# Performance work log

Hardware: AMD Instinct MI355X
Metric: run time of the kernel (lower is better)

The kernel has to match this reference:

```python
import jax, jax.numpy as jnp
import numpy as np

N, H, W = 128, 64, 64
CH_I, CH_H, CH_Q = 2, 150, 10
N_ACT = 8


def conv3x3(x, w):
    # x: [N,H,W,Cin], w: [3,3,Cin,Cout], 'same' padding, stride 1
    return jax.lax.conv_general_dilated(
        x, w, window_strides=(1, 1), padding='SAME',
        dimension_numbers=('NHWC', 'HWIO', 'NHWC'))


def setup_inputs() -> dict:
    key = jax.random.key(0)
    ks = jax.random.split(key, 9)
    std = 0.01
    x = jax.random.normal(ks[0], (N, H, W, CH_I), dtype=jnp.float32)
    S1 = jax.random.randint(ks[1], (N,), 0, H, dtype=jnp.int32)
    S2 = jax.random.randint(ks[2], (N,), 0, W, dtype=jnp.int32)
    w0 = std * jax.random.normal(ks[3], (3, 3, CH_I, CH_H), dtype=jnp.float32)
    b0 = jnp.zeros((CH_H,), dtype=jnp.float32)
    w_r = std * jax.random.normal(ks[4], (3, 3, CH_H, 1), dtype=jnp.float32)
    w_q = std * jax.random.normal(ks[5], (3, 3, 2, CH_Q), dtype=jnp.float32)
    w_sw = std * jax.random.normal(ks[6], (3, 3, 2, CH_Q), dtype=jnp.float32)
    w_sw2 = std * jax.random.normal(ks[7], (3, 3, 2, CH_Q), dtype=jnp.float32)
    w_dense = std * jax.random.normal(ks[8], (CH_Q, N_ACT), dtype=jnp.float32)
    return {"x": x, "S1": S1, "S2": S2, "VInum": 36,
            "w0": w0, "b0": b0, "w_r": w_r, "w_q": w_q,
            "w_sw": w_sw, "w_sw2": w_sw2, "w_dense": w_dense}


def reference(x, S1, S2, VInum, w0, b0, w_r, w_q, w_sw, w_sw2, w_dense):
    k = int(VInum)
    h = conv3x3(x, w0) + b0                      # [N,H,W,ch_h]
    r = conv3x3(h, w_r)                          # [N,H,W,1] reward map
    v = jnp.zeros_like(r)
    # first VI step uses conv2 weights
    q = conv3x3(jnp.concatenate([r, v], axis=3), w_q)
    v = jnp.max(q, axis=3, keepdims=True)
    # k-1 shared-weight value-iteration steps
    def body(v, _):
        q = conv3x3(jnp.concatenate([r, v], axis=3), w_sw)
        return jnp.max(q, axis=3, keepdims=True), None
    v, _ = jax.lax.scan(body, v, None, length=k - 1)
    # final step with second shared-weight conv
    q = conv3x3(jnp.concatenate([r, v], axis=3), w_sw2)  # [N,H,W,ch_q]
    # attention: gather Q values at state (S1,S2) per batch element
    q_out = q[jnp.arange(q.shape[0]), S1, S2]            # [N,ch_q]
    logits = q_out @ w_dense                             # [N,8]
    prob_actions = jax.nn.softmax(logits, axis=-1)
    return (logits, prob_actions, q, q_out)
```

## Files before the change

kernel.cpp:

```cpp
#include <hip/hip_runtime.h>
#include <math.h>


typedef float v2f __attribute__((ext_vector_type(2)));

static __device__ __forceinline__ v2f splat2(float s) { v2f r; r.x = s; r.y = s; return r; }
static __device__ __forceinline__ v2f pkfma(v2f w, float v, v2f a) {
#if __has_builtin(__builtin_elementwise_fma)
    return __builtin_elementwise_fma(w, splat2(v), a);
#else
    v2f r; r.x = fmaf(w.x, v, a.x); r.y = fmaf(w.y, v, a.y); return r;
#endif
}
static __device__ __forceinline__ v2f pkmax(v2f a, v2f b) {
#if __has_builtin(__builtin_elementwise_max)
    return __builtin_elementwise_max(a, b);
#else
    v2f r; r.x = fmaxf(a.x, b.x); r.y = fmaxf(a.y, b.y); return r;
#endif
}

#define DPP_SHR1 0x138
#define DPP_SHL1 0x130
template <int CTRL>
static __device__ __forceinline__ float dppsh(float v) {
    return __int_as_float(__builtin_amdgcn_update_dpp(
        0, __float_as_int(v), CTRL, 0xF, 0xF, false));
}

#define XROW 69
#define RROW 68

__global__ void
__attribute__((amdgpu_flat_work_group_size(1024, 1024)))
__attribute__((amdgpu_waves_per_eu(4, 4)))
vin_kernel(const float* __restrict__ x,
           const int* __restrict__ S1,
           const int* __restrict__ S2,
           const int* __restrict__ VInum,
           const float* __restrict__ w0,
           const float* __restrict__ b0,
           const float* __restrict__ w_r,
           const float* __restrict__ w_q,
           const float* __restrict__ w_sw,
           const float* __restrict__ w_sw2,
           const float* __restrict__ w_dense,
           float* __restrict__ out) {
    const int b = blockIdx.x;
    const int t = threadIdx.x;

    __shared__ float xs0[68 * XROW];
    __shared__ float xs1[68 * XROW];
    __shared__ float rs[66 * RROW];
    __shared__ float wtA[1620];
    __shared__ float Pp[450];
    __shared__ float Bt[90];
    __shared__ float Bv[9];
    __shared__ float W5c[459];
    __shared__ float exT[2][17][64];
    __shared__ float exB[2][17][64];
    __shared__ float qsel[10];

    for (int i = t; i < 68 * XROW; i += 1024) { xs0[i] = 0.f; xs1[i] = 0.f; }
    for (int i = t; i < 66 * RROW; i += 1024) rs[i] = 0.f;
    for (int i = t; i < 2 * 17 * 64; i += 1024) {
        ((float*)exT)[i] = 0.f; ((float*)exB)[i] = 0.f;
    }
    if (t < 450) Pp[t] = 0.f;
    __syncthreads();

    const int row = t >> 4;
    const int cb  = (t & 15) << 2;

    {
        const float* xb = x + (size_t)b * 64 * 64 * 2;
        const float4* xp = (const float4*)(xb + (row * 64 + cb) * 2);
        #pragma unroll
        for (int g = 0; g < 2; ++g) {
            float4 v4 = xp[g];
            int px = cb + g * 2;
            xs0[(row + 2) * XROW + px + 2] = v4.x;
            xs1[(row + 2) * XROW + px + 2] = v4.y;
            xs0[(row + 2) * XROW + px + 3] = v4.z;
            xs1[(row + 2) * XROW + px + 3] = v4.w;
        }
    }
    for (int idx = t; idx < 1620; idx += 1024) {
        int entry = idx / 10, ch = idx - entry * 10;
        int d = entry / 18, rem = entry % 18;
        int uu = rem >> 1, ci = rem & 1;
        int c0 = ch * 15;
        const float* wr = w_r + d * 150;
        const float* wp = w0 + (uu * 2 + ci) * 150;
        float s = 0.f;
        for (int c = c0; c < c0 + 15; ++c) s += wr[c] * wp[c];
        wtA[idx] = s;
    }
    if (t < 90) {
        int d = t / 10, ch = t - d * 10, c0 = ch * 15;
        float s = 0.f;
        for (int c = c0; c < c0 + 15; ++c) s += w_r[d * 150 + c] * b0[c];
        Bt[t] = s;
    }
    __syncthreads();
    if (t < 162) {
        float s = 0.f;
        #pragma unroll
        for (int i = 0; i < 10; ++i) s += wtA[t * 10 + i];
        int d = t / 18, rem = t % 18;
        int uu = rem >> 1, ci = rem & 1;
        int dy = d / 3 - 1, dx = d % 3 - 1;
        int uy = uu / 3 - 1, ux = uu % 3 - 1;
        int eidx = (dy + uy + 2) * 5 + (dx + ux + 2);
        Pp[d * 50 + eidx * 2 + ci] = s;
    } else if (t >= 256 && t < 265) {
        int d = t - 256;
        float s = 0.f;
        #pragma unroll
        for (int i = 0; i < 10; ++i) s += Bt[d * 10 + i];
        Bv[d] = s;
    }
    __syncthreads();
    if (t < 459) {
        int cls = t / 51, j = t - cls * 51;
        int cy = cls / 3, cx = cls % 3;
        float s = 0.f;
        #pragma unroll
        for (int d = 0; d < 9; ++d) {
            int dy = d / 3 - 1, dx = d % 3 - 1;
            bool ok = (cy == 0 || (cy == 1 ? dy >= 0 : dy <= 0)) &&
                      (cx == 0 || (cx == 1 ? dx >= 0 : dx <= 0));
            if (ok) s += (j < 50) ? Pp[d * 50 + j] : Bv[d];
        }
        W5c[t] = s;
    }
    __syncthreads();

    {
        int cy = (row == 0) ? 1 : (row == 63) ? 2 : 0;
        #pragma unroll
        for (int p = 0; p < 4; ++p) {
            int xx = cb + p;
            int cx = (xx == 0) ? 1 : (xx == 63) ? 2 : 0;
            const float* Wp = &W5c[(cy * 3 + cx) * 51];
            float acc = Wp[50];
            #pragma unroll
            for (int e = 0; e < 25; ++e) {
                int xi = (row + e / 5) * XROW + (xx + e % 5);
                acc = fmaf(xs0[xi], Wp[e * 2], acc);
                acc = fmaf(xs1[xi], Wp[e * 2 + 1], acc);
            }
            rs[(row + 1) * RROW + xx + 2] = acc;
        }
    }
    __syncthreads();

    const int c  = t & 63;
    const int w  = t >> 6;
    const int r0 = w << 2;
    const int upSlot = (w == 0)  ? 16 : w - 1;
    const int dnSlot = (w == 15) ? 16 : w + 1;
    const int K = VInum[0];

    v2f Rsw2[4][5];
    float vprev[4];
    float RC[6], RL[6], RR[6];
    #pragma unroll
    for (int j = 0; j < 6; ++j) RC[j] = rs[(r0 + j) * RROW + c + 2];
    #pragma unroll
    for (int j = 0; j < 6; ++j) { RL[j] = dppsh<DPP_SHR1>(RC[j]); RR[j] = dppsh<DPP_SHL1>(RC[j]); }
    {
        float vmax[4];
        #pragma unroll
        for (int a = 0; a < 10; ++a) {
            #pragma unroll
            for (int i = 0; i < 4; ++i) {
                float accR = 0.f, accQ = 0.f;
                #pragma unroll
                for (int d = 0; d < 9; ++d) {
                    const int dy = d / 3, dx = d % 3;
                    const float rv = (dx == 0 ? RL : dx == 1 ? RC : RR)[i + dy];
                    accR = fmaf(w_sw[d * 20 + a], rv, accR);
                    accQ = fmaf(w_q[d * 20 + a],  rv, accQ);
                }
                if (a & 1) Rsw2[i][a >> 1].y = accR; else Rsw2[i][a >> 1].x = accR;
                vmax[i] = (a == 0) ? accQ : fmaxf(vmax[i], accQ);
            }
        }
        exT[1][w][c] = vmax[0];
        exB[1][w][c] = vmax[3];
        #pragma unroll
        for (int i = 0; i < 4; ++i) vprev[i] = vmax[i];
    }
    __syncthreads();

    const float* wsv = w_sw + 10;
    for (int k = 2; k <= K; ++k) {
        const int pr = (k - 1) & 1, pw = k & 1;
        float VC[6], VL[6], VR[6];
        VC[0] = exB[pr][upSlot][c];
        VC[5] = exT[pr][dnSlot][c];
        #pragma unroll
        for (int i = 0; i < 4; ++i) VC[i + 1] = vprev[i];
        #pragma unroll
        for (int j = 0; j < 6; ++j) { VL[j] = dppsh<DPP_SHR1>(VC[j]); VR[j] = dppsh<DPP_SHL1>(VC[j]); }

        v2f acc[4][5];
        #pragma unroll
        for (int ap = 0; ap < 5; ++ap) {
            #pragma unroll
            for (int d = 0; d < 9; ++d) {
                v2f w2; w2.x = wsv[d * 20 + 2 * ap]; w2.y = wsv[d * 20 + 2 * ap + 1];
                const int dy = d / 3, dx = d % 3;
                const float* S = (dx == 0) ? VL : (dx == 1) ? VC : VR;
                #pragma unroll
                for (int i = 0; i < 4; ++i)
                    acc[i][ap] = (d == 0) ? pkfma(w2, S[i + dy], Rsw2[i][ap])
                                          : pkfma(w2, S[i + dy], acc[i][ap]);
            }
        }
        float vnew[4];
        #pragma unroll
        for (int i = 0; i < 4; ++i) {
            v2f m2 = acc[i][0];
            #pragma unroll
            for (int ap = 1; ap < 5; ++ap) m2 = pkmax(m2, acc[i][ap]);
            vnew[i] = fmaxf(m2.x, m2.y);
        }
        exT[pw][w][c] = vnew[0];
        exB[pw][w][c] = vnew[3];
        #pragma unroll
        for (int i = 0; i < 4; ++i) vprev[i] = vnew[i];
        __syncthreads();
    }

    const int s1 = S1[b], s2 = S2[b];
    {
        const int pK = K & 1;
        float VC[6], VL[6], VR[6];
        VC[0] = exB[pK][upSlot][c];
        VC[5] = exT[pK][dnSlot][c];
        #pragma unroll
        for (int i = 0; i < 4; ++i) VC[i + 1] = vprev[i];
        #pragma unroll
        for (int j = 0; j < 6; ++j) { VL[j] = dppsh<DPP_SHR1>(VC[j]); VR[j] = dppsh<DPP_SHL1>(VC[j]); }

        float qv[4][10];
        #pragma unroll
        for (int a = 0; a < 10; ++a) {
            #pragma unroll
            for (int i = 0; i < 4; ++i) {
                float acc = 0.f;
                #pragma unroll
                for (int d = 0; d < 9; ++d) {
                    const int dy = d / 3, dx = d % 3;
                    acc = fmaf(w_sw2[d * 20 + a],
                               (dx == 0 ? RL : dx == 1 ? RC : RR)[i + dy], acc);
                    acc = fmaf(w_sw2[d * 20 + 10 + a],
                               (dx == 0 ? VL : dx == 1 ? VC : VR)[i + dy], acc);
                }
                qv[i][a] = acc;
            }
        }
        #pragma unroll
        for (int i = 0; i < 4; ++i) {
            float2* qp = (float2*)(out + 2048 +
                          ((size_t)((b * 64 + r0 + i) * 64 + c)) * 10);
            #pragma unroll
            for (int g = 0; g < 5; ++g)
                qp[g] = make_float2(qv[i][2 * g], qv[i][2 * g + 1]);
        }
        if (c == s2) {
            #pragma unroll
            for (int i = 0; i < 4; ++i)
                if (s1 == r0 + i) {
                    #pragma unroll
                    for (int a = 0; a < 10; ++a) qsel[a] = qv[i][a];
                }
        }
    }
    __syncthreads();

    if (t == 0) {
        float logits[8];
        float m = -1e30f;
        #pragma unroll
        for (int j = 0; j < 8; ++j) {
            float s = 0.f;
            #pragma unroll
            for (int a = 0; a < 10; ++a) s += qsel[a] * w_dense[a * 8 + j];
            logits[j] = s;
            m = fmaxf(m, s);
        }
        float sum = 0.f;
        float e[8];
        #pragma unroll
        for (int j = 0; j < 8; ++j) { e[j] = expf(logits[j] - m); sum += e[j]; }
        float inv = 1.f / sum;
        #pragma unroll
        for (int j = 0; j < 8; ++j) {
            out[b * 8 + j] = logits[j];
            out[1024 + b * 8 + j] = e[j] * inv;
        }
    }
    if (t < 10) out[5244928 + b * 10 + t] = qsel[t];
}

extern "C" void kernel_launch(void* const* d_in, const int* in_sizes, int n_in,
                              void* d_out, int out_size, void* d_ws, size_t ws_size,
                              hipStream_t stream) {
    const float* x      = (const float*)d_in[0];
    const int*   S1     = (const int*)d_in[1];
    const int*   S2     = (const int*)d_in[2];
    const int*   VInum  = (const int*)d_in[3];
    const float* w0     = (const float*)d_in[4];
    const float* b0     = (const float*)d_in[5];
    const float* w_r    = (const float*)d_in[6];
    const float* w_q    = (const float*)d_in[7];
    const float* w_sw   = (const float*)d_in[8];
    const float* w_sw2  = (const float*)d_in[9];
    const float* w_dense= (const float*)d_in[10];
    float* out = (float*)d_out;

    vin_kernel<<<128, 1024, 0, stream>>>(x, S1, S2, VInum, w0, b0, w_r, w_q,
                                         w_sw, w_sw2, w_dense, out);
}
```

Before: 171.4 us.

## Halve block size to 512 threads, 8 rows per thread, weights in registers

Each thread now computes 8 rows of the value-iteration map instead of 4, with 512 threads per block and 2 waves per SIMD. This lowers the halo overhead per row (shared-memory exchange and DPP shifts) and means fewer waves take part in each per-iteration barrier. The shared-weight conv weights are also loaded once into 45 packed register pairs rather than re-read from memory on every iteration. In exchange, fewer resident waves are left to hide latency, and register pressure rises a lot, which could cause spills.

After: 176.2 us. 1.03x slower.

```diff
diff --git a/kernel.cpp b/kernel.cpp
--- a/kernel.cpp
+++ b/kernel.cpp
@@ -32,8 +32,8 @@
 #define RROW 68
 
 __global__ void
-__attribute__((amdgpu_flat_work_group_size(1024, 1024)))
-__attribute__((amdgpu_waves_per_eu(4, 4)))
+__attribute__((amdgpu_flat_work_group_size(512, 512)))
+__attribute__((amdgpu_waves_per_eu(2, 2)))
 vin_kernel(const float* __restrict__ x,
            const int* __restrict__ S1,
            const int* __restrict__ S2,
@@ -57,26 +57,26 @@
     __shared__ float Bt[90];
     __shared__ float Bv[9];
     __shared__ float W5c[459];
-    __shared__ float exT[2][17][64];
-    __shared__ float exB[2][17][64];
+    __shared__ float exT[2][9][64];
+    __shared__ float exB[2][9][64];
     __shared__ float qsel[10];
 
-    for (int i = t; i < 68 * XROW; i += 1024) { xs0[i] = 0.f; xs1[i] = 0.f; }
-    for (int i = t; i < 66 * RROW; i += 1024) rs[i] = 0.f;
-    for (int i = t; i < 2 * 17 * 64; i += 1024) {
+    for (int i = t; i < 68 * XROW; i += 512) { xs0[i] = 0.f; xs1[i] = 0.f; }
+    for (int i = t; i < 66 * RROW; i += 512) rs[i] = 0.f;
+    for (int i = t; i < 2 * 9 * 64; i += 512) {
         ((float*)exT)[i] = 0.f; ((float*)exB)[i] = 0.f;
     }
     if (t < 450) Pp[t] = 0.f;
     __syncthreads();
 
-    const int row = t >> 4;
-    const int cb  = (t & 15) << 2;
+    const int row = t >> 3;
+    const int cb  = (t & 7) << 3;
 
     {
         const float* xb = x + (size_t)b * 64 * 64 * 2;
         const float4* xp = (const float4*)(xb + (row * 64 + cb) * 2);
         #pragma unroll
-        for (int g = 0; g < 2; ++g) {
+        for (int g = 0; g < 4; ++g) {
             float4 v4 = xp[g];
             int px = cb + g * 2;
             xs0[(row + 2) * XROW + px + 2] = v4.x;
@@ -85,7 +85,7 @@
             xs1[(row + 2) * XROW + px + 3] = v4.w;
         }
     }
-    for (int idx = t; idx < 1620; idx += 1024) {
+    for (int idx = t; idx < 1620; idx += 512) {
         int entry = idx / 10, ch = idx - entry * 10;
         int d = entry / 18, rem = entry % 18;
         int uu = rem >> 1, ci = rem & 1;
@@ -139,7 +139,7 @@
     {
         int cy = (row == 0) ? 1 : (row == 63) ? 2 : 0;
         #pragma unroll
-        for (int p = 0; p < 4; ++p) {
+        for (int p = 0; p < 8; ++p) {
             int xx = cb + p;
             int cx = (xx == 0) ? 1 : (xx == 63) ? 2 : 0;
             const float* Wp = &W5c[(cy * 3 + cx) * 51];
@@ -157,24 +157,26 @@
 
     const int c  = t & 63;
     const int w  = t >> 6;
-    const int r0 = w << 2;
-    const int upSlot = (w == 0)  ? 16 : w - 1;
-    const int dnSlot = (w == 15) ? 16 : w + 1;
+    const int r0 = w << 3;
+    const int upSlot = (w == 0) ? 8 : w - 1;
+    const int dnSlot = (w == 7) ? 8 : w + 1;
     const int K = VInum[0];
 
-    v2f Rsw2[4][5];
-    float vprev[4];
-    float RC[6], RL[6], RR[6];
-    #pragma unroll
-    for (int j = 0; j < 6; ++j) RC[j] = rs[(r0 + j) * RROW + c + 2];
-    #pragma unroll
-    for (int j = 0; j < 6; ++j) { RL[j] = dppsh<DPP_SHR1>(RC[j]); RR[j] = dppsh<DPP_SHL1>(RC[j]); }
+    v2f Rsw2[8][5];
+    float vprev[8];
     {
-        float vmax[4];
+        float RC[10], RL[10], RR[10];
+        #pragma unroll
+        for (int j = 0; j < 10; ++j) RC[j] = rs[(r0 + j) * RROW + c + 2];
+        #pragma unroll
+        for (int j = 0; j < 10; ++j) {
+            RL[j] = dppsh<DPP_SHR1>(RC[j]); RR[j] = dppsh<DPP_SHL1>(RC[j]);
+        }
+        float vmax[8];
         #pragma unroll
         for (int a = 0; a < 10; ++a) {
             #pragma unroll
-            for (int i = 0; i < 4; ++i) {
+            for (int i = 0; i < 8; ++i) {
                 float accR = 0.f, accQ = 0.f;
                 #pragma unroll
                 for (int d = 0; d < 9; ++d) {
@@ -188,68 +190,108 @@
             }
         }
         exT[1][w][c] = vmax[0];
-        exB[1][w][c] = vmax[3];
-        #pragma unroll
-        for (int i = 0; i < 4; ++i) vprev[i] = vmax[i];
-    }
-    __syncthreads();
-
-    const float* wsv = w_sw + 10;
+        exB[1][w][c] = vmax[7];
+        #pragma unroll
+        for (int i = 0; i < 8; ++i) vprev[i] = vmax[i];
+    }
+
+    v2f wv[45];
+    #pragma unroll
+    for (int i = 0; i < 45; ++i) {
+        const int d = i / 5, ap = i - d * 5;
+        v2f v; v.x = w_sw[d * 20 + 10 + 2 * ap]; v.y = w_sw[d * 20 + 10 + 2 * ap + 1];
+        asm volatile("" : "+v"(v));
+        wv[i] = v;
+    }
+    __syncthreads();
+
     for (int k = 2; k <= K; ++k) {
         const int pr = (k - 1) & 1, pw = k & 1;
-        float VC[6], VL[6], VR[6];
+        float VC[10], VL[10], VR[10];
         VC[0] = exB[pr][upSlot][c];
-        VC[5] = exT[pr][dnSlot][c];
-        #pragma unroll
-        for (int i = 0; i < 4; ++i) VC[i + 1] = vprev[i];
-        #pragma unroll
-        for (int j = 0; j < 6; ++j) { VL[j] = dppsh<DPP_SHR1>(VC[j]); VR[j] = dppsh<DPP_SHL1>(VC[j]); }
-
-        v2f acc[4][5];
-        #pragma unroll
-        for (int ap = 0; ap < 5; ++ap) {
-            #pragma unroll
-            for (int d = 0; d < 9; ++d) {
-                v2f w2; w2.x = wsv[d * 20 + 2 * ap]; w2.y = wsv[d * 20 + 2 * ap + 1];
-                const int dy = d / 3, dx = d % 3;
-                const float* S = (dx == 0) ? VL : (dx == 1) ? VC : VR;
-                #pragma unroll
-                for (int i = 0; i < 4; ++i)
-                    acc[i][ap] = (d == 0) ? pkfma(w2, S[i + dy], Rsw2[i][ap])
-                                          : pkfma(w2, S[i + dy], acc[i][ap]);
-            }
-        }
-        float vnew[4];
-        #pragma unroll
-        for (int i = 0; i < 4; ++i) {
-            v2f m2 = acc[i][0];
-            #pragma unroll
-            for (int ap = 1; ap < 5; ++ap) m2 = pkmax(m2, acc[i][ap]);
-            vnew[i] = fmaxf(m2.x, m2.y);
+        VC[9] = exT[pr][dnSlot][c];
+        #pragma unroll
+        for (int i = 0; i < 8; ++i) VC[i + 1] = vprev[i];
+        #pragma unroll
+        for (int j = 0; j < 10; ++j) {
+            VL[j] = dppsh<DPP_SHR1>(VC[j]); VR[j] = dppsh<DPP_SHL1>(VC[j]);
+        }
+
+        float vnew[8];
+        {
+            v2f acc[4][5];
+            #pragma unroll
+            for (int ap = 0; ap < 5; ++ap) {
+                #pragma unroll
+                for (int d = 0; d < 9; ++d) {
+                    const int dy = d / 3, dx = d % 3;
+                    const float* S = (dx == 0) ? VL : (dx == 1) ? VC : VR;
+                    v2f w2 = wv[d * 5 + ap];
+                    #pragma unroll
+                    for (int i = 0; i < 4; ++i)
+                        acc[i][ap] = (d == 0) ? pkfma(w2, S[i + dy], Rsw2[i][ap])
+                                              : pkfma(w2, S[i + dy], acc[i][ap]);
+                }
+            }
+            #pragma unroll
+            for (int i = 0; i < 4; ++i) {
+                v2f m2 = acc[i][0];
+                #pragma unroll
+                for (int ap = 1; ap < 5; ++ap) m2 = pkmax(m2, acc[i][ap]);
+                vnew[i] = fmaxf(m2.x, m2.y);
+            }
+        }
+        {
+            v2f acc[4][5];
+            #pragma unroll
+            for (int ap = 0; ap < 5; ++ap) {
+                #pragma unroll
+                for (int d = 0; d < 9; ++d) {
+                    const int dy = d / 3, dx = d % 3;
+                    const float* S = (dx == 0) ? VL : (dx == 1) ? VC : VR;
+                    v2f w2 = wv[d * 5 + ap];
+                    #pragma unroll
+                    for (int i = 0; i < 4; ++i)
+                        acc[i][ap] = (d == 0) ? pkfma(w2, S[i + 4 + dy], Rsw2[i + 4][ap])
+                                              : pkfma(w2, S[i + 4 + dy], acc[i][ap]);
+                }
+            }
+            #pragma unroll
+            for (int i = 0; i < 4; ++i) {
+                v2f m2 = acc[i][0];
+                #pragma unroll
+                for (int ap = 1; ap < 5; ++ap) m2 = pkmax(m2, acc[i][ap]);
+                vnew[i + 4] = fmaxf(m2.x, m2.y);
+            }
         }
         exT[pw][w][c] = vnew[0];
-        exB[pw][w][c] = vnew[3];
-        #pragma unroll
-        for (int i = 0; i < 4; ++i) vprev[i] = vnew[i];
+        exB[pw][w][c] = vnew[7];
+        #pragma unroll
+        for (int i = 0; i < 8; ++i) vprev[i] = vnew[i];
         __syncthreads();
     }
 
     const int s1 = S1[b], s2 = S2[b];
     {
         const int pK = K & 1;
-        float VC[6], VL[6], VR[6];
+        float RC[10], RL[10], RR[10], VC[10], VL[10], VR[10];
+        #pragma unroll
+        for (int j = 0; j < 10; ++j) RC[j] = rs[(r0 + j) * RROW + c + 2];
         VC[0] = exB[pK][upSlot][c];
-        VC[5] = exT[pK][dnSlot][c];
-        #pragma unroll
-        for (int i = 0; i < 4; ++i) VC[i + 1] = vprev[i];
-        #pragma unroll
-        for (int j = 0; j < 6; ++j) { VL[j] = dppsh<DPP_SHR1>(VC[j]); VR[j] = dppsh<DPP_SHL1>(VC[j]); }
-
-        float qv[4][10];
+        VC[9] = exT[pK][dnSlot][c];
+        #pragma unroll
+        for (int i = 0; i < 8; ++i) VC[i + 1] = vprev[i];
+        #pragma unroll
+        for (int j = 0; j < 10; ++j) {
+            RL[j] = dppsh<DPP_SHR1>(RC[j]); RR[j] = dppsh<DPP_SHL1>(RC[j]);
+            VL[j] = dppsh<DPP_SHR1>(VC[j]); VR[j] = dppsh<DPP_SHL1>(VC[j]);
+        }
+
+        float qv[8][10];
         #pragma unroll
         for (int a = 0; a < 10; ++a) {
             #pragma unroll
-            for (int i = 0; i < 4; ++i) {
+            for (int i = 0; i < 8; ++i) {
                 float acc = 0.f;
                 #pragma unroll
                 for (int d = 0; d < 9; ++d) {
@@ -263,7 +305,7 @@
             }
         }
         #pragma unroll
-        for (int i = 0; i < 4; ++i) {
+        for (int i = 0; i < 8; ++i) {
             float2* qp = (float2*)(out + 2048 +
                           ((size_t)((b * 64 + r0 + i) * 64 + c)) * 10);
             #pragma unroll
@@ -272,7 +314,7 @@
         }
         if (c == s2) {
             #pragma unroll
-            for (int i = 0; i < 4; ++i)
+            for (int i = 0; i < 8; ++i)
                 if (s1 == r0 + i) {
                     #pragma unroll
                     for (int a = 0; a < 10; ++a) qsel[a] = qv[i][a];
@@ -322,6 +364,6 @@
     const float* w_dense= (const float*)d_in[10];
     float* out = (float*)d_out;
 
-    vin_kernel<<<128, 1024, 0, stream>>>(x, S1, S2, VInum, w0, b0, w_r, w_q,
-                                         w_sw, w_sw2, w_dense, out);
-}
+    vin_kernel<<<128, 512, 0, stream>>>(x, S1, S2, VInum, w0, b0, w_r, w_q,
+                                        w_sw, w_sw2, w_dense, out);
+}
```

## Fuse two value-iteration steps per barrier using two-row halo recomputation

Applied to the files above, without the earlier changes.

Each wave now exchanges a two-row halo, packed as float2, and computes two VI steps per synchronization. It first computes 6 rows (its own 4 plus one redundant halo row on each side), then the 4 owned rows from those, which halves the number of __syncthreads barriers in the iterative loop. The price is roughly 50% redundant FMA work in the first step of each pair and more live registers (6x5 precomputed reward terms, 6-row accumulators). Per-action accumulation is split into chunks to limit register pressure, and an odd leftover step is handled separately.

Measured after the change: 183.0 us. 1.07x slower.

```diff
diff --git a/kernel.cpp b/kernel.cpp
--- a/kernel.cpp
+++ b/kernel.cpp
@@ -49,22 +49,23 @@
     const int b = blockIdx.x;
     const int t = threadIdx.x;
 
-    __shared__ float xs0[68 * XROW];
-    __shared__ float xs1[68 * XROW];
-    __shared__ float rs[66 * RROW];
-    __shared__ float wtA[1620];
-    __shared__ float Pp[450];
-    __shared__ float Bt[90];
-    __shared__ float Bv[9];
-    __shared__ float W5c[459];
-    __shared__ float exT[2][17][64];
-    __shared__ float exB[2][17][64];
-    __shared__ float qsel[10];
+    __shared__ float  xs0[68 * XROW];
+    __shared__ float  xs1[68 * XROW];
+    __shared__ float  rs[66 * RROW];
+    __shared__ float  wtA[1620];
+    __shared__ float  Pp[450];
+    __shared__ float  Bt[90];
+    __shared__ float  Bv[9];
+    __shared__ float  W5c[459];
+    __shared__ float2 exU[2][17][64];
+    __shared__ float2 exD[2][17][64];
+    __shared__ float  qsel[10];
 
     for (int i = t; i < 68 * XROW; i += 1024) { xs0[i] = 0.f; xs1[i] = 0.f; }
     for (int i = t; i < 66 * RROW; i += 1024) rs[i] = 0.f;
     for (int i = t; i < 2 * 17 * 64; i += 1024) {
-        ((float*)exT)[i] = 0.f; ((float*)exB)[i] = 0.f;
+        ((float2*)exU)[i] = make_float2(0.f, 0.f);
+        ((float2*)exD)[i] = make_float2(0.f, 0.f);
     }
     if (t < 450) Pp[t] = 0.f;
     __syncthreads();
@@ -162,89 +163,260 @@
     const int dnSlot = (w == 15) ? 16 : w + 1;
     const int K = VInum[0];
 
-    v2f Rsw2[4][5];
+    v2f Rsw2[6][5];
     float vprev[4];
-    float RC[6], RL[6], RR[6];
-    #pragma unroll
-    for (int j = 0; j < 6; ++j) RC[j] = rs[(r0 + j) * RROW + c + 2];
-    #pragma unroll
-    for (int j = 0; j < 6; ++j) { RL[j] = dppsh<DPP_SHR1>(RC[j]); RR[j] = dppsh<DPP_SHL1>(RC[j]); }
     {
+        float RC2[8], RL2[8], RR2[8];
+        #pragma unroll
+        for (int j = 0; j < 8; ++j) {
+            int grow = r0 - 2 + j;
+            int gcl = grow < -1 ? -1 : (grow > 64 ? 64 : grow);
+            RC2[j] = rs[(gcl + 1) * RROW + c + 2];
+        }
+        #pragma unroll
+        for (int j = 0; j < 8; ++j) {
+            RL2[j] = dppsh<DPP_SHR1>(RC2[j]); RR2[j] = dppsh<DPP_SHL1>(RC2[j]);
+        }
         float vmax[4];
         #pragma unroll
         for (int a = 0; a < 10; ++a) {
             #pragma unroll
-            for (int i = 0; i < 4; ++i) {
-                float accR = 0.f, accQ = 0.f;
-                #pragma unroll
-                for (int d = 0; d < 9; ++d) {
-                    const int dy = d / 3, dx = d % 3;
-                    const float rv = (dx == 0 ? RL : dx == 1 ? RC : RR)[i + dy];
+            for (int i = 0; i < 6; ++i) {
+                float accR = 0.f;
+                #pragma unroll
+                for (int d = 0; d < 9; ++d) {
+                    const int dy = d / 3, dx = d % 3;
+                    const float rv = (dx == 0 ? RL2 : dx == 1 ? RC2 : RR2)[i + dy];
                     accR = fmaf(w_sw[d * 20 + a], rv, accR);
-                    accQ = fmaf(w_q[d * 20 + a],  rv, accQ);
                 }
                 if (a & 1) Rsw2[i][a >> 1].y = accR; else Rsw2[i][a >> 1].x = accR;
-                vmax[i] = (a == 0) ? accQ : fmaxf(vmax[i], accQ);
-            }
-        }
-        exT[1][w][c] = vmax[0];
-        exB[1][w][c] = vmax[3];
-        #pragma unroll
-        for (int i = 0; i < 4; ++i) vprev[i] = vmax[i];
-    }
-    __syncthreads();
-
-    const float* wsv = w_sw + 10;
-    for (int k = 2; k <= K; ++k) {
-        const int pr = (k - 1) & 1, pw = k & 1;
-        float VC[6], VL[6], VR[6];
-        VC[0] = exB[pr][upSlot][c];
-        VC[5] = exT[pr][dnSlot][c];
-        #pragma unroll
-        for (int i = 0; i < 4; ++i) VC[i + 1] = vprev[i];
-        #pragma unroll
-        for (int j = 0; j < 6; ++j) { VL[j] = dppsh<DPP_SHR1>(VC[j]); VR[j] = dppsh<DPP_SHL1>(VC[j]); }
-
-        v2f acc[4][5];
-        #pragma unroll
-        for (int ap = 0; ap < 5; ++ap) {
+            }
+            #pragma unroll
+            for (int j = 0; j < 4; ++j) {
+                float accQ = 0.f;
+                #pragma unroll
+                for (int d = 0; d < 9; ++d) {
+                    const int dy = d / 3, dx = d % 3;
+                    const float rv = (dx == 0 ? RL2 : dx == 1 ? RC2 : RR2)[j + 1 + dy];
+                    accQ = fmaf(w_q[d * 20 + a], rv, accQ);
+                }
+                vmax[j] = (a == 0) ? accQ : fmaxf(vmax[j], accQ);
+            }
+        }
+        exU[0][w][c] = make_float2(vmax[0], vmax[1]);
+        exD[0][w][c] = make_float2(vmax[2], vmax[3]);
+        #pragma unroll
+        for (int j = 0; j < 4; ++j) vprev[j] = vmax[j];
+    }
+
+    int cur = 0;
+    int k = 2;
+    for (; k + 1 <= K; k += 2) {
+        __syncthreads();
+        float2 gU = exD[cur][upSlot][c];
+        float2 gD = exU[cur][dnSlot][c];
+        float VC[8];
+        VC[0] = gU.x; VC[1] = gU.y;
+        #pragma unroll
+        for (int j = 0; j < 4; ++j) VC[2 + j] = vprev[j];
+        VC[6] = gD.x; VC[7] = gD.y;
+
+        float vA[6];
+        v2f vmA[6];
+        {
+            float VL[8], VR[8];
+            #pragma unroll
+            for (int j = 0; j < 8; ++j) { VL[j] = dppsh<DPP_SHR1>(VC[j]); VR[j] = dppsh<DPP_SHL1>(VC[j]); }
+            v2f acc[6][2];
+            #pragma unroll
+            for (int ap = 0; ap < 2; ++ap)
+                #pragma unroll
+                for (int d = 0; d < 9; ++d) {
+                    v2f w2; w2.x = w_sw[d * 20 + 10 + 2 * ap]; w2.y = w_sw[d * 20 + 10 + 2 * ap + 1];
+                    const int dy = d / 3, dx = d % 3;
+                    const float* S = (dx == 0) ? VL : (dx == 1) ? VC : VR;
+                    #pragma unroll
+                    for (int i = 0; i < 6; ++i)
+                        acc[i][ap] = (d == 0) ? pkfma(w2, S[i + dy], Rsw2[i][ap])
+                                              : pkfma(w2, S[i + dy], acc[i][ap]);
+                }
+            #pragma unroll
+            for (int i = 0; i < 6; ++i) vmA[i] = pkmax(acc[i][0], acc[i][1]);
+        }
+        {
+            float VL[8], VR[8];
+            #pragma unroll
+            for (int j = 0; j < 8; ++j) { VL[j] = dppsh<DPP_SHR1>(VC[j]); VR[j] = dppsh<DPP_SHL1>(VC[j]); }
+            v2f acc[6][2];
+            #pragma unroll
+            for (int ap = 0; ap < 2; ++ap)
+                #pragma unroll
+                for (int d = 0; d < 9; ++d) {
+                    const int apx = 2 + ap;
+                    v2f w2; w2.x = w_sw[d * 20 + 10 + 2 * apx]; w2.y = w_sw[d * 20 + 10 + 2 * apx + 1];
+                    const int dy = d / 3, dx = d % 3;
+                    const float* S = (dx == 0) ? VL : (dx == 1) ? VC : VR;
+                    #pragma unroll
+                    for (int i = 0; i < 6; ++i)
+                        acc[i][ap] = (d == 0) ? pkfma(w2, S[i + dy], Rsw2[i][apx])
+                                              : pkfma(w2, S[i + dy], acc[i][ap]);
+                }
+            #pragma unroll
+            for (int i = 0; i < 6; ++i) vmA[i] = pkmax(pkmax(vmA[i], acc[i][0]), acc[i][1]);
+        }
+        {
+            float VL[8], VR[8];
+            #pragma unroll
+            for (int j = 0; j < 8; ++j) { VL[j] = dppsh<DPP_SHR1>(VC[j]); VR[j] = dppsh<DPP_SHL1>(VC[j]); }
+            v2f acc[6];
             #pragma unroll
             for (int d = 0; d < 9; ++d) {
-                v2f w2; w2.x = wsv[d * 20 + 2 * ap]; w2.y = wsv[d * 20 + 2 * ap + 1];
+                v2f w2; w2.x = w_sw[d * 20 + 10 + 8]; w2.y = w_sw[d * 20 + 10 + 9];
                 const int dy = d / 3, dx = d % 3;
                 const float* S = (dx == 0) ? VL : (dx == 1) ? VC : VR;
                 #pragma unroll
-                for (int i = 0; i < 4; ++i)
-                    acc[i][ap] = (d == 0) ? pkfma(w2, S[i + dy], Rsw2[i][ap])
-                                          : pkfma(w2, S[i + dy], acc[i][ap]);
-            }
-        }
-        float vnew[4];
-        #pragma unroll
-        for (int i = 0; i < 4; ++i) {
-            v2f m2 = acc[i][0];
-            #pragma unroll
-            for (int ap = 1; ap < 5; ++ap) m2 = pkmax(m2, acc[i][ap]);
-            vnew[i] = fmaxf(m2.x, m2.y);
-        }
-        exT[pw][w][c] = vnew[0];
-        exB[pw][w][c] = vnew[3];
-        #pragma unroll
-        for (int i = 0; i < 4; ++i) vprev[i] = vnew[i];
+                for (int i = 0; i < 6; ++i)
+                    acc[i] = (d == 0) ? pkfma(w2, S[i + dy], Rsw2[i][4])
+                                      : pkfma(w2, S[i + dy], acc[i]);
+            }
+            #pragma unroll
+            for (int i = 0; i < 6; ++i) vmA[i] = pkmax(vmA[i], acc[i]);
+        }
+        #pragma unroll
+        for (int i = 0; i < 6; ++i) vA[i] = fmaxf(vmA[i].x, vmA[i].y);
+        if (w == 0)  vA[0] = 0.f;
+        if (w == 15) vA[5] = 0.f;
+
+        float vB[4];
+        v2f vmB[4];
+        {
+            float VL[6], VR[6];
+            #pragma unroll
+            for (int j = 0; j < 6; ++j) { VL[j] = dppsh<DPP_SHR1>(vA[j]); VR[j] = dppsh<DPP_SHL1>(vA[j]); }
+            v2f acc[4][2];
+            #pragma unroll
+            for (int ap = 0; ap < 2; ++ap)
+                #pragma unroll
+                for (int d = 0; d < 9; ++d) {
+                    v2f w2; w2.x = w_sw[d * 20 + 10 + 2 * ap]; w2.y = w_sw[d * 20 + 10 + 2 * ap + 1];
+                    const int dy = d / 3, dx = d % 3;
+                    const float* S = (dx == 0) ? VL : (dx == 1) ? vA : VR;
+                    #pragma unroll
+                    for (int j = 0; j < 4; ++j)
+                        acc[j][ap] = (d == 0) ? pkfma(w2, S[j + dy], Rsw2[j + 1][ap])
+                                              : pkfma(w2, S[j + dy], acc[j][ap]);
+                }
+            #pragma unroll
+            for (int j = 0; j < 4; ++j) vmB[j] = pkmax(acc[j][0], acc[j][1]);
+        }
+        {
+            float VL[6], VR[6];
+            #pragma unroll
+            for (int j = 0; j < 6; ++j) { VL[j] = dppsh<DPP_SHR1>(vA[j]); VR[j] = dppsh<DPP_SHL1>(vA[j]); }
+            v2f acc[4][2];
+            #pragma unroll
+            for (int ap = 0; ap < 2; ++ap)
+                #pragma unroll
+                for (int d = 0; d < 9; ++d) {
+                    const int apx = 2 + ap;
+                    v2f w2; w2.x = w_sw[d * 20 + 10 + 2 * apx]; w2.y = w_sw[d * 20 + 10 + 2 * apx + 1];
+                    const int dy = d / 3, dx = d % 3;
+                    const float* S = (dx == 0) ? VL : (dx == 1) ? vA : VR;
+                    #pragma unroll
+                    for (int j = 0; j < 4; ++j)
+                        acc[j][ap] = (d == 0) ? pkfma(w2, S[j + dy], Rsw2[j + 1][apx])
+                                              : pkfma(w2, S[j + dy], acc[j][ap]);
+                }
+            #pragma unroll
+            for (int j = 0; j < 4; ++j) vmB[j] = pkmax(pkmax(vmB[j], acc[j][0]), acc[j][1]);
+        }
+        {
+            float VL[6], VR[6];
+            #pragma unroll
+            for (int j = 0; j < 6; ++j) { VL[j] = dppsh<DPP_SHR1>(vA[j]); VR[j] = dppsh<DPP_SHL1>(vA[j]); }
+            v2f acc[4];
+            #pragma unroll
+            for (int d = 0; d < 9; ++d) {
+                v2f w2; w2.x = w_sw[d * 20 + 10 + 8]; w2.y = w_sw[d * 20 + 10 + 9];
+                const int dy = d / 3, dx = d % 3;
+                const float* S = (dx == 0) ? VL : (dx == 1) ? vA : VR;
+                #pragma unroll
+                for (int j = 0; j < 4; ++j)
+                    acc[j] = (d == 0) ? pkfma(w2, S[j + dy], Rsw2[j + 1][4])
+                                      : pkfma(w2, S[j + dy], acc[j]);
+            }
+            #pragma unroll
+            for (int j = 0; j < 4; ++j) vmB[j] = pkmax(vmB[j], acc[j]);
+        }
+        #pragma unroll
+        for (int j = 0; j < 4; ++j) vB[j] = fmaxf(vmB[j].x, vmB[j].y);
+
+        int nxt = cur ^ 1;
+        exU[nxt][w][c] = make_float2(vB[0], vB[1]);
+        exD[nxt][w][c] = make_float2(vB[2], vB[3]);
+        #pragma unroll
+        for (int j = 0; j < 4; ++j) vprev[j] = vB[j];
+        cur = nxt;
+    }
+
+    if (k <= K) {
         __syncthreads();
-    }
-
+        float gu = exD[cur][upSlot][c].y;
+        float gd = exU[cur][dnSlot][c].x;
+        float VC1[6];
+        VC1[0] = gu;
+        #pragma unroll
+        for (int j = 0; j < 4; ++j) VC1[1 + j] = vprev[j];
+        VC1[5] = gd;
+        float VL1[6], VR1[6];
+        #pragma unroll
+        for (int j = 0; j < 6; ++j) { VL1[j] = dppsh<DPP_SHR1>(VC1[j]); VR1[j] = dppsh<DPP_SHL1>(VC1[j]); }
+        v2f acc[4][5];
+        #pragma unroll
+        for (int ap = 0; ap < 5; ++ap)
+            #pragma unroll
+            for (int d = 0; d < 9; ++d) {
+                v2f w2; w2.x = w_sw[d * 20 + 10 + 2 * ap]; w2.y = w_sw[d * 20 + 10 + 2 * ap + 1];
+                const int dy = d / 3, dx = d % 3;
+                const float* S = (dx == 0) ? VL1 : (dx == 1) ? VC1 : VR1;
+                #pragma unroll
+                for (int j = 0; j < 4; ++j)
+                    acc[j][ap] = (d == 0) ? pkfma(w2, S[j + dy], Rsw2[j + 1][ap])
+                                          : pkfma(w2, S[j + dy], acc[j][ap]);
+            }
+        float vB[4];
+        #pragma unroll
+        for (int j = 0; j < 4; ++j) {
+            v2f m2 = acc[j][0];
+            #pragma unroll
+            for (int ap = 1; ap < 5; ++ap) m2 = pkmax(m2, acc[j][ap]);
+            vB[j] = fmaxf(m2.x, m2.y);
+        }
+        int nxt = cur ^ 1;
+        exU[nxt][w][c] = make_float2(vB[0], vB[1]);
+        exD[nxt][w][c] = make_float2(vB[2], vB[3]);
+        #pragma unroll
+        for (int j = 0; j < 4; ++j) vprev[j] = vB[j];
+        cur = nxt;
+    }
+
+    __syncthreads();
     const int s1 = S1[b], s2 = S2[b];
     {
-        const int pK = K & 1;
-        float VC[6], VL[6], VR[6];
-        VC[0] = exB[pK][upSlot][c];
-        VC[5] = exT[pK][dnSlot][c];
-        #pragma unroll
-        for (int i = 0; i < 4; ++i) VC[i + 1] = vprev[i];
-        #pragma unroll
-        for (int j = 0; j < 6; ++j) { VL[j] = dppsh<DPP_SHR1>(VC[j]); VR[j] = dppsh<DPP_SHL1>(VC[j]); }
-
+        float gu = exD[cur][upSlot][c].y;
+        float gd = exU[cur][dnSlot][c].x;
+        float VCf[6], VLf[6], VRf[6], RCf[6], RLf[6], RRf[6];
+        VCf[0] = gu;
+        #pragma unroll
+        for (int j = 0; j < 4; ++j) VCf[1 + j] = vprev[j];
+        VCf[5] = gd;
+        #pragma unroll
+        for (int j = 0; j < 6; ++j) RCf[j] = rs[(r0 + j) * RROW + c + 2];
+        #pragma unroll
+        for (int j = 0; j < 6; ++j) {
+            VLf[j] = dppsh<DPP_SHR1>(VCf[j]); VRf[j] = dppsh<DPP_SHL1>(VCf[j]);
+            RLf[j] = dppsh<DPP_SHR1>(RCf[j]); RRf[j] = dppsh<DPP_SHL1>(RCf[j]);
+        }
         float qv[4][10];
         #pragma unroll
         for (int a = 0; a < 10; ++a) {
@@ -255,9 +427,9 @@
                 for (int d = 0; d < 9; ++d) {
                     const int dy = d / 3, dx = d % 3;
                     acc = fmaf(w_sw2[d * 20 + a],
-                               (dx == 0 ? RL : dx == 1 ? RC : RR)[i + dy], acc);
+                               (dx == 0 ? RLf : dx == 1 ? RCf : RRf)[i + dy], acc);
                     acc = fmaf(w_sw2[d * 20 + 10 + a],
-                               (dx == 0 ? VL : dx == 1 ? VC : VR)[i + dy], acc);
+                               (dx == 0 ? VLf : dx == 1 ? VCf : VRf)[i + dy], acc);
                 }
                 qv[i][a] = acc;
             }
```

## Split each image across two blocks with global-memory halo exchange per VI step

Applied to the files above, without the earlier changes.

Each batch image is now handled by two 512-thread blocks, each owning 32 rows, so the grid has 256 blocks instead of 128 and more CUs are in use. The neighbouring blocks swap boundary value rows every value-iteration step through a workspace in global memory, using release/acquire flags and spin-waits. Block indices are mapped so both halves of an image land on the same XCD, which keeps the exchange in a shared L2. This adds a memset launch and cross-block spin synchronisation on each of the ~36 steps, and it depends on both blocks being resident at the same time.

New measurement: 428.9 us. 2.5x slower.

```diff
diff --git a/kernel.cpp b/kernel.cpp
--- a/kernel.cpp
+++ b/kernel.cpp
@@ -29,11 +29,13 @@
 }
 
 #define XROW 69
-#define RROW 68
+#define VROW 67
+#define XS_ROWS 38
+#define RS_ROWS 34
 
 __global__ void
-__attribute__((amdgpu_flat_work_group_size(1024, 1024)))
-__attribute__((amdgpu_waves_per_eu(4, 4)))
+__attribute__((amdgpu_flat_work_group_size(512, 512)))
+__attribute__((amdgpu_waves_per_eu(2, 2)))
 vin_kernel(const float* __restrict__ x,
            const int* __restrict__ S1,
            const int* __restrict__ S2,
@@ -45,128 +47,135 @@
            const float* __restrict__ w_sw,
            const float* __restrict__ w_sw2,
            const float* __restrict__ w_dense,
-           float* __restrict__ out) {
-    const int b = blockIdx.x;
+           float* __restrict__ out,
+           void* __restrict__ ws) {
+    const int g = blockIdx.x;
     const int t = threadIdx.x;
-
-    __shared__ float xs0[68 * XROW];
-    __shared__ float xs1[68 * XROW];
-    __shared__ float rs[66 * RROW];
+    const int xcd  = g & 7;
+    const int slot = g >> 3;
+    const int b    = xcd * 16 + (slot >> 1);
+    const int h    = slot & 1;
+    const int s    = h << 5;
+
+    int*   F   = (int*)ws;
+    float* Hdn = (float*)ws + 8192;
+    float* Hup = Hdn + 128 * 2 * 64;
+    int* Fdn = &F[(b * 2 + 0) * 32];
+    int* Fup = &F[(b * 2 + 1) * 32];
+
+    __shared__ float xs0[XS_ROWS * XROW];
+    __shared__ float xs1[XS_ROWS * XROW];
+    __shared__ float rs[RS_ROWS * VROW];
     __shared__ float wtA[1620];
     __shared__ float Pp[450];
     __shared__ float Bt[90];
     __shared__ float Bv[9];
     __shared__ float W5c[459];
-    __shared__ float exT[2][17][64];
-    __shared__ float exB[2][17][64];
+    __shared__ float exT[2][9][64];
+    __shared__ float exB[2][9][64];
     __shared__ float qsel[10];
 
-    for (int i = t; i < 68 * XROW; i += 1024) { xs0[i] = 0.f; xs1[i] = 0.f; }
-    for (int i = t; i < 66 * RROW; i += 1024) rs[i] = 0.f;
-    for (int i = t; i < 2 * 17 * 64; i += 1024) {
+    for (int i = t; i < XS_ROWS * XROW; i += 512) { xs0[i] = 0.f; xs1[i] = 0.f; }
+    for (int i = t; i < RS_ROWS * VROW; i += 512) rs[i] = 0.f;
+    for (int i = t; i < 2 * 9 * 64; i += 512) {
         ((float*)exT)[i] = 0.f; ((float*)exB)[i] = 0.f;
     }
     if (t < 450) Pp[t] = 0.f;
     __syncthreads();
 
-    const int row = t >> 4;
-    const int cb  = (t & 15) << 2;
-
-    {
-        const float* xb = x + (size_t)b * 64 * 64 * 2;
-        const float4* xp = (const float4*)(xb + (row * 64 + cb) * 2);
-        #pragma unroll
-        for (int g = 0; g < 2; ++g) {
-            float4 v4 = xp[g];
-            int px = cb + g * 2;
-            xs0[(row + 2) * XROW + px + 2] = v4.x;
-            xs1[(row + 2) * XROW + px + 2] = v4.y;
-            xs0[(row + 2) * XROW + px + 3] = v4.z;
-            xs1[(row + 2) * XROW + px + 3] = v4.w;
-        }
-    }
-    for (int idx = t; idx < 1620; idx += 1024) {
+    for (int i = t; i < XS_ROWS * 32; i += 512) {
+        int xl = i >> 5, grp = i & 31;
+        int gx = s - 3 + xl;
+        if (gx < 0 || gx > 63) continue;
+        float4 v4 = *(const float4*)(x + ((size_t)(b * 64 + gx) * 64 + grp * 2) * 2);
+        int px = grp * 2;
+        xs0[xl * XROW + px + 2] = v4.x; xs1[xl * XROW + px + 2] = v4.y;
+        xs0[xl * XROW + px + 3] = v4.z; xs1[xl * XROW + px + 3] = v4.w;
+    }
+    for (int idx = t; idx < 1620; idx += 512) {
         int entry = idx / 10, ch = idx - entry * 10;
         int d = entry / 18, rem = entry % 18;
         int uu = rem >> 1, ci = rem & 1;
         int c0 = ch * 15;
         const float* wr = w_r + d * 150;
         const float* wp = w0 + (uu * 2 + ci) * 150;
-        float s = 0.f;
-        for (int c = c0; c < c0 + 15; ++c) s += wr[c] * wp[c];
-        wtA[idx] = s;
+        float ssum = 0.f;
+        for (int c = c0; c < c0 + 15; ++c) ssum += wr[c] * wp[c];
+        wtA[idx] = ssum;
     }
     if (t < 90) {
         int d = t / 10, ch = t - d * 10, c0 = ch * 15;
-        float s = 0.f;
-        for (int c = c0; c < c0 + 15; ++c) s += w_r[d * 150 + c] * b0[c];
-        Bt[t] = s;
+        float ssum = 0.f;
+        for (int c = c0; c < c0 + 15; ++c) ssum += w_r[d * 150 + c] * b0[c];
+        Bt[t] = ssum;
     }
     __syncthreads();
     if (t < 162) {
-        float s = 0.f;
-        #pragma unroll
-        for (int i = 0; i < 10; ++i) s += wtA[t * 10 + i];
+        float ssum = 0.f;
+        #pragma unroll
+        for (int i = 0; i < 10; ++i) ssum += wtA[t * 10 + i];
         int d = t / 18, rem = t % 18;
         int uu = rem >> 1, ci = rem & 1;
         int dy = d / 3 - 1, dx = d % 3 - 1;
         int uy = uu / 3 - 1, ux = uu % 3 - 1;
         int eidx = (dy + uy + 2) * 5 + (dx + ux + 2);
-        Pp[d * 50 + eidx * 2 + ci] = s;
+        Pp[d * 50 + eidx * 2 + ci] = ssum;
     } else if (t >= 256 && t < 265) {
         int d = t - 256;
-        float s = 0.f;
-        #pragma unroll
-        for (int i = 0; i < 10; ++i) s += Bt[d * 10 + i];
-        Bv[d] = s;
+        float ssum = 0.f;
+        #pragma unroll
+        for (int i = 0; i < 10; ++i) ssum += Bt[d * 10 + i];
+        Bv[d] = ssum;
     }
     __syncthreads();
     if (t < 459) {
         int cls = t / 51, j = t - cls * 51;
         int cy = cls / 3, cx = cls % 3;
-        float s = 0.f;
+        float ssum = 0.f;
         #pragma unroll
         for (int d = 0; d < 9; ++d) {
             int dy = d / 3 - 1, dx = d % 3 - 1;
             bool ok = (cy == 0 || (cy == 1 ? dy >= 0 : dy <= 0)) &&
                       (cx == 0 || (cx == 1 ? dx >= 0 : dx <= 0));
-            if (ok) s += (j < 50) ? Pp[d * 50 + j] : Bv[d];
-        }
-        W5c[t] = s;
-    }
-    __syncthreads();
-
-    {
-        int cy = (row == 0) ? 1 : (row == 63) ? 2 : 0;
-        #pragma unroll
-        for (int p = 0; p < 4; ++p) {
-            int xx = cb + p;
-            int cx = (xx == 0) ? 1 : (xx == 63) ? 2 : 0;
-            const float* Wp = &W5c[(cy * 3 + cx) * 51];
-            float acc = Wp[50];
-            #pragma unroll
-            for (int e = 0; e < 25; ++e) {
-                int xi = (row + e / 5) * XROW + (xx + e % 5);
-                acc = fmaf(xs0[xi], Wp[e * 2], acc);
-                acc = fmaf(xs1[xi], Wp[e * 2 + 1], acc);
-            }
-            rs[(row + 1) * RROW + xx + 2] = acc;
-        }
-    }
-    __syncthreads();
-
-    const int c  = t & 63;
-    const int w  = t >> 6;
-    const int r0 = w << 2;
-    const int upSlot = (w == 0)  ? 16 : w - 1;
-    const int dnSlot = (w == 15) ? 16 : w + 1;
+            if (ok) ssum += (j < 50) ? Pp[d * 50 + j] : Bv[d];
+        }
+        W5c[t] = ssum;
+    }
+    __syncthreads();
+
+    for (int i = t; i < RS_ROWS * 64; i += 512) {
+        int ri = i >> 6;
+        int c  = i & 63;
+        int gy = s + ri - 1;
+        if (gy < 0 || gy > 63) continue;
+        int cy = (gy == 0) ? 1 : (gy == 63) ? 2 : 0;
+        int cx = (c == 0) ? 1 : (c == 63) ? 2 : 0;
+        const float* Wp = &W5c[(cy * 3 + cx) * 51];
+        float acc = Wp[50];
+        #pragma unroll
+        for (int e = 0; e < 25; ++e) {
+            int xi = (ri + e / 5) * XROW + (c + e % 5);
+            acc = fmaf(xs0[xi], Wp[e * 2], acc);
+            acc = fmaf(xs1[xi], Wp[e * 2 + 1], acc);
+        }
+        rs[ri * VROW + (c + 1)] = acc;
+    }
+    __syncthreads();
+
+    const int c   = t & 63;
+    const int w   = t >> 6;
+    const int lr0 = w << 2;
+    const int upSlot = (w == 0) ? 8 : w - 1;
+    const int dnSlot = (w == 7) ? 8 : w + 1;
+    const bool ghostTop = (h == 1 && w == 0);
+    const bool ghostBot = (h == 0 && w == 7);
     const int K = VInum[0];
 
     v2f Rsw2[4][5];
     float vprev[4];
     float RC[6], RL[6], RR[6];
     #pragma unroll
-    for (int j = 0; j < 6; ++j) RC[j] = rs[(r0 + j) * RROW + c + 2];
+    for (int j = 0; j < 6; ++j) RC[j] = rs[(lr0 + j) * VROW + c + 1];
     #pragma unroll
     for (int j = 0; j < 6; ++j) { RL[j] = dppsh<DPP_SHR1>(RC[j]); RR[j] = dppsh<DPP_SHL1>(RC[j]); }
     {
@@ -189,17 +198,42 @@
         }
         exT[1][w][c] = vmax[0];
         exB[1][w][c] = vmax[3];
+        if (ghostBot) {
+            __hip_atomic_store(&Hdn[(b * 2 + 1) * 64 + c], vmax[3],
+                               __ATOMIC_RELAXED, __HIP_MEMORY_SCOPE_AGENT);
+            __threadfence();
+            if (c == 0) __hip_atomic_store(Fdn, 1, __ATOMIC_RELEASE, __HIP_MEMORY_SCOPE_AGENT);
+        }
+        if (ghostTop) {
+            __hip_atomic_store(&Hup[(b * 2 + 1) * 64 + c], vmax[0],
+                               __ATOMIC_RELAXED, __HIP_MEMORY_SCOPE_AGENT);
+            __threadfence();
+            if (c == 0) __hip_atomic_store(Fup, 1, __ATOMIC_RELEASE, __HIP_MEMORY_SCOPE_AGENT);
+        }
         #pragma unroll
         for (int i = 0; i < 4; ++i) vprev[i] = vmax[i];
     }
     __syncthreads();
 
-    const float* wsv = w_sw + 10;
     for (int k = 2; k <= K; ++k) {
         const int pr = (k - 1) & 1, pw = k & 1;
+        float vTop, vBot;
+        if (ghostTop) {
+            while (__hip_atomic_load(Fdn, __ATOMIC_ACQUIRE, __HIP_MEMORY_SCOPE_AGENT) < k - 1) {}
+            vTop = __hip_atomic_load(&Hdn[(b * 2 + pr) * 64 + c],
+                                     __ATOMIC_RELAXED, __HIP_MEMORY_SCOPE_AGENT);
+        } else {
+            vTop = exB[pr][upSlot][c];
+        }
+        if (ghostBot) {
+            while (__hip_atomic_load(Fup, __ATOMIC_ACQUIRE, __HIP_MEMORY_SCOPE_AGENT) < k - 1) {}
+            vBot = __hip_atomic_load(&Hup[(b * 2 + pr) * 64 + c],
+                                     __ATOMIC_RELAXED, __HIP_MEMORY_SCOPE_AGENT);
+        } else {
+            vBot = exT[pr][dnSlot][c];
+        }
         float VC[6], VL[6], VR[6];
-        VC[0] = exB[pr][upSlot][c];
-        VC[5] = exT[pr][dnSlot][c];
+        VC[0] = vTop; VC[5] = vBot;
         #pragma unroll
         for (int i = 0; i < 4; ++i) VC[i + 1] = vprev[i];
         #pragma unroll
@@ -210,7 +244,7 @@
         for (int ap = 0; ap < 5; ++ap) {
             #pragma unroll
             for (int d = 0; d < 9; ++d) {
-                v2f w2; w2.x = wsv[d * 20 + 2 * ap]; w2.y = wsv[d * 20 + 2 * ap + 1];
+                v2f w2; w2.x = w_sw[d * 20 + 10 + 2 * ap]; w2.y = w_sw[d * 20 + 10 + 2 * ap + 1];
                 const int dy = d / 3, dx = d % 3;
                 const float* S = (dx == 0) ? VL : (dx == 1) ? VC : VR;
                 #pragma unroll
@@ -229,6 +263,18 @@
         }
         exT[pw][w][c] = vnew[0];
         exB[pw][w][c] = vnew[3];
+        if (ghostBot) {
+            __hip_atomic_store(&Hdn[(b * 2 + pw) * 64 + c], vnew[3],
+                               __ATOMIC_RELAXED, __HIP_MEMORY_SCOPE_AGENT);
+            __threadfence();
+            if (c == 0) __hip_atomic_store(Fdn, k, __ATOMIC_RELEASE, __HIP_MEMORY_SCOPE_AGENT);
+        }
+        if (ghostTop) {
+            __hip_atomic_store(&Hup[(b * 2 + pw) * 64 + c], vnew[0],
+                               __ATOMIC_RELAXED, __HIP_MEMORY_SCOPE_AGENT);
+            __threadfence();
+            if (c == 0) __hip_atomic_store(Fup, k, __ATOMIC_RELEASE, __HIP_MEMORY_SCOPE_AGENT);
+        }
         #pragma unroll
         for (int i = 0; i < 4; ++i) vprev[i] = vnew[i];
         __syncthreads();
@@ -237,9 +283,23 @@
     const int s1 = S1[b], s2 = S2[b];
     {
         const int pK = K & 1;
+        float vTop, vBot;
+        if (ghostTop) {
+            while (__hip_atomic_load(Fdn, __ATOMIC_ACQUIRE, __HIP_MEMORY_SCOPE_AGENT) < K) {}
+            vTop = __hip_atomic_load(&Hdn[(b * 2 + pK) * 64 + c],
+                                     __ATOMIC_RELAXED, __HIP_MEMORY_SCOPE_AGENT);
+        } else {
+            vTop = exB[pK][upSlot][c];
+        }
+        if (ghostBot) {
+            while (__hip_atomic_load(Fup, __ATOMIC_ACQUIRE, __HIP_MEMORY_SCOPE_AGENT) < K) {}
+            vBot = __hip_atomic_load(&Hup[(b * 2 + pK) * 64 + c],
+                                     __ATOMIC_RELAXED, __HIP_MEMORY_SCOPE_AGENT);
+        } else {
+            vBot = exT[pK][dnSlot][c];
+        }
         float VC[6], VL[6], VR[6];
-        VC[0] = exB[pK][upSlot][c];
-        VC[5] = exT[pK][dnSlot][c];
+        VC[0] = vTop; VC[5] = vBot;
         #pragma unroll
         for (int i = 0; i < 4; ++i) VC[i + 1] = vprev[i];
         #pragma unroll
@@ -265,15 +325,15 @@
         #pragma unroll
         for (int i = 0; i < 4; ++i) {
             float2* qp = (float2*)(out + 2048 +
-                          ((size_t)((b * 64 + r0 + i) * 64 + c)) * 10);
-            #pragma unroll
-            for (int g = 0; g < 5; ++g)
-                qp[g] = make_float2(qv[i][2 * g], qv[i][2 * g + 1]);
+                          ((size_t)((b * 64 + s + lr0 + i) * 64 + c)) * 10);
+            #pragma unroll
+            for (int gq = 0; gq < 5; ++gq)
+                qp[gq] = make_float2(qv[i][2 * gq], qv[i][2 * gq + 1]);
         }
         if (c == s2) {
             #pragma unroll
             for (int i = 0; i < 4; ++i)
-                if (s1 == r0 + i) {
+                if (s1 == s + lr0 + i) {
                     #pragma unroll
                     for (int a = 0; a < 10; ++a) qsel[a] = qv[i][a];
                 }
@@ -281,29 +341,31 @@
     }
     __syncthreads();
 
-    if (t == 0) {
-        float logits[8];
-        float m = -1e30f;
-        #pragma unroll
-        for (int j = 0; j < 8; ++j) {
-            float s = 0.f;
-            #pragma unroll
-            for (int a = 0; a < 10; ++a) s += qsel[a] * w_dense[a * 8 + j];
-            logits[j] = s;
-            m = fmaxf(m, s);
-        }
-        float sum = 0.f;
-        float e[8];
-        #pragma unroll
-        for (int j = 0; j < 8; ++j) { e[j] = expf(logits[j] - m); sum += e[j]; }
-        float inv = 1.f / sum;
-        #pragma unroll
-        for (int j = 0; j < 8; ++j) {
-            out[b * 8 + j] = logits[j];
-            out[1024 + b * 8 + j] = e[j] * inv;
-        }
-    }
-    if (t < 10) out[5244928 + b * 10 + t] = qsel[t];
+    if ((s1 >> 5) == h) {
+        if (t == 0) {
+            float logits[8];
+            float m = -1e30f;
+            #pragma unroll
+            for (int j = 0; j < 8; ++j) {
+                float ssum = 0.f;
+                #pragma unroll
+                for (int a = 0; a < 10; ++a) ssum += qsel[a] * w_dense[a * 8 + j];
+                logits[j] = ssum;
+                m = fmaxf(m, ssum);
+            }
+            float sum = 0.f;
+            float e[8];
+            #pragma unroll
+            for (int j = 0; j < 8; ++j) { e[j] = expf(logits[j] - m); sum += e[j]; }
+            float inv = 1.f / sum;
+            #pragma unroll
+            for (int j = 0; j < 8; ++j) {
+                out[b * 8 + j] = logits[j];
+                out[1024 + b * 8 + j] = e[j] * inv;
+            }
+        }
+        if (t < 10) out[5244928 + b * 10 + t] = qsel[t];
+    }
 }
 
 extern "C" void kernel_launch(void* const* d_in, const int* in_sizes, int n_in,
@@ -322,6 +384,7 @@
     const float* w_dense= (const float*)d_in[10];
     float* out = (float*)d_out;
 
-    vin_kernel<<<128, 1024, 0, stream>>>(x, S1, S2, VInum, w0, b0, w_r, w_q,
-                                         w_sw, w_sw2, w_dense, out);
-}
+    hipMemsetAsync(d_ws, 0, 8192 * sizeof(int), stream);
+    vin_kernel<<<256, 512, 0, stream>>>(x, S1, S2, VInum, w0, b0, w_r, w_q,
+                                        w_sw, w_sw2, w_dense, out, d_ws);
+}
```
